# Kernel optimization log

Measured on AMD Instinct MI355X. Metric: run time of the kernel, lower is better.

The kernel has to match this reference:

```python
import jax, jax.numpy as jnp
import numpy as np

D, H, E, K, DF = 1024, 16, 8, 2, 4096
HD = D // H


def setup_inputs() -> dict:
    key = jax.random.key(0)
    ks = jax.random.split(key, 16)
    s = 0.02
    return {
        "x": jax.random.normal(ks[0], (8, 1024, D), jnp.float32),
        "ln1_g": jnp.ones((D,), jnp.float32),
        "ln1_b": jnp.zeros((D,), jnp.float32),
        "Wqkv": jax.random.normal(ks[1], (D, 3 * D), jnp.float32) * s,
        "bqkv": jnp.zeros((3 * D,), jnp.float32),
        "Wo": jax.random.normal(ks[2], (D, D), jnp.float32) * s,
        "bo": jnp.zeros((D,), jnp.float32),
        "ln2_g": jnp.ones((D,), jnp.float32),
        "ln2_b": jnp.zeros((D,), jnp.float32),
        "Wr": jax.random.normal(ks[3], (D, E), jnp.float32) * s,
        "W1": jax.random.normal(ks[4], (E, D, DF), jnp.float32) * s,
        "b1": jnp.zeros((E, DF), jnp.float32),
        "W2": jax.random.normal(ks[5], (E, DF, D), jnp.float32) * s,
        "b2": jnp.zeros((E, D), jnp.float32),
    }


def _ln(x, g, b, eps=1e-5):
    mu = jnp.mean(x, axis=-1, keepdims=True)
    var = jnp.var(x, axis=-1, keepdims=True)
    return (x - mu) * jax.lax.rsqrt(var + eps) * g + b


def reference(x, ln1_g, ln1_b, Wqkv, bqkv, Wo, bo, ln2_g, ln2_b, Wr, W1, b1, W2, b2):
    B, S, _ = x.shape
    # ---- pre-norm multi-head attention ----
    n1 = _ln(x, ln1_g, ln1_b)
    qkv = n1 @ Wqkv + bqkv  # [B,S,3D]
    q, k, v = jnp.split(qkv, 3, axis=-1)
    q = q.reshape(B, S, H, HD).transpose(0, 2, 1, 3)
    k = k.reshape(B, S, H, HD).transpose(0, 2, 1, 3)
    v = v.reshape(B, S, H, HD).transpose(0, 2, 1, 3)
    scores = jnp.einsum("bhqd,bhkd->bhqk", q, k) / np.sqrt(HD).astype(np.float32)
    attn = jax.nn.softmax(scores, axis=-1)
    ao = jnp.einsum("bhqk,bhkd->bhqd", attn, v)
    ao = ao.transpose(0, 2, 1, 3).reshape(B, S, D) @ Wo + bo
    x = x + ao  # residual (dropout=0)

    # ---- pre-norm MoE FFN ----
    n2 = _ln(x, ln2_g, ln2_b).reshape(B * S, D)  # [T,D]
    logits = n2 @ Wr  # [T,E]
    probs = jax.nn.softmax(logits, axis=-1)
    topv, topi = jax.lax.top_k(probs, K)  # [T,K]
    topv = topv / jnp.sum(topv, axis=-1, keepdims=True)
    onehot = jax.nn.one_hot(topi, E, dtype=probs.dtype)  # [T,K,E]
    gates = jnp.einsum("tke,tk->te", onehot, topv)  # dense sparse gates [T,E]

    # dense dispatch: each expert's FFN weighted by its gate (zero for unrouted)
    moe = jnp.zeros_like(n2)
    for e in range(E):
        h = jax.nn.gelu(n2 @ W1[e] + b1[e])
        moe = moe + gates[:, e:e + 1] * (h @ W2[e] + b2[e])
    x = x + moe.reshape(B, S, D)

    # load-balancing aux loss: E * sum(frac_routed_e * mean_prob_e)
    frac = jnp.mean(jnp.sum(onehot, axis=1), axis=0) / K  # [E]
    aux = E * jnp.sum(frac * jnp.mean(probs, axis=0))
    return x, aux
```

## Files before the change

kernel.cpp:

```cpp
#include <hip/hip_runtime.h>
#include <cstdint>
#include <cstddef>

using u16 = unsigned short;
using u32 = unsigned int;
typedef __attribute__((ext_vector_type(8))) short bf16x8;
typedef __attribute__((ext_vector_type(4))) float f32x4;

#define T_TOK 8192
#define SEQ   1024
#define NHEAD 16

__device__ __forceinline__ u16 f2b(float f) {
  u32 u = __float_as_uint(f);
  u32 r = (u + 0x7FFFu + ((u >> 16) & 1u)) >> 16;
  return (u16)r;
}
__device__ __forceinline__ float b2f(u16 u) {
  return __uint_as_float(((u32)u) << 16);
}
__device__ __forceinline__ u32 pk_bf16(float a, float b) {
  u32 r;
  asm("v_cvt_pk_bf16_f32 %0, %1, %2" : "=v"(r) : "v"(a), "v"(b));
  return r;
}

__global__ __launch_bounds__(256)
void k_cast_transpose(const float* __restrict__ in, u16* __restrict__ out, int R, int C) {
  __shared__ float tile[32][33];
  int bc = blockIdx.x * 32, br = blockIdx.y * 32;
  size_t bofs = (size_t)blockIdx.z * R * C;
  in += bofs; out += bofs;
  int tx = threadIdx.x, ty = threadIdx.y;
  for (int i = 0; i < 32; i += 8)
    tile[ty + i][tx] = in[(size_t)(br + ty + i) * C + bc + tx];
  __syncthreads();
  for (int i = 0; i < 32; i += 8)
    out[(size_t)(bc + ty + i) * R + br + tx] = f2b(tile[tx][ty + i]);
}

__global__ __launch_bounds__(256)
void k_ln(const float* __restrict__ x, const float* __restrict__ g, const float* __restrict__ b,
          u16* __restrict__ out) {
  int row = blockIdx.x, t = threadIdx.x;
  float4 v = ((const float4*)(x + (size_t)row * 1024))[t];
  float s  = v.x + v.y + v.z + v.w;
  float ss = v.x * v.x + v.y * v.y + v.z * v.z + v.w * v.w;
  for (int d = 1; d < 64; d <<= 1) { s += __shfl_xor(s, d); ss += __shfl_xor(ss, d); }
  __shared__ float sm[8];
  int w = t >> 6, lane = t & 63;
  if (lane == 0) { sm[w] = s; sm[4 + w] = ss; }
  __syncthreads();
  s = sm[0] + sm[1] + sm[2] + sm[3];
  ss = sm[4] + sm[5] + sm[6] + sm[7];
  float mu = s * (1.f / 1024.f);
  float var = ss * (1.f / 1024.f) - mu * mu;
  float inv = rsqrtf(var + 1e-5f);
  float4 gv = ((const float4*)g)[t];
  float4 bv = ((const float4*)b)[t];
  u32 lo = pk_bf16((v.x - mu) * inv * gv.x + bv.x, (v.y - mu) * inv * gv.y + bv.y);
  u32 hi = pk_bf16((v.z - mu) * inv * gv.z + bv.z, (v.w - mu) * inv * gv.w + bv.w);
  u32* dst = (u32*)(out + (size_t)row * 1024 + t * 4);
  dst[0] = lo; dst[1] = hi;
}

template<int MODE, bool EXPERT, bool GATHER>
__global__ __launch_bounds__(256)
void k_gemm(const u16* __restrict__ A, const u16* __restrict__ BT,
            const float* __restrict__ bias, const float* __restrict__ res,
            void* __restrict__ Cout, int M, int N, int Kd, int ldA,
            const int* __restrict__ off, const int* __restrict__ rows) {
  int nx = gridDim.x, ny = gridDim.y;
  int rid = blockIdx.x + nx * (blockIdx.y + ny * blockIdx.z);
  int z, bx, by;
  if (EXPERT) {
    z = rid & 7;
    int inner = rid >> 3;
    by = inner % ny;
    bx = inner / ny;
  } else {
    z = 0;
    int xcd = rid & 7;
    int inner = rid >> 3;
    bx = inner % nx;
    by = (inner / nx) * 8 + xcd;
  }
  int m_base = 0, M_local = M;
  if (EXPERT) { m_base = off[z]; M_local = off[z + 1] - m_base; }
  if (by * 128 >= M_local) return;
  if (EXPERT) { BT += (size_t)z * N * Kd; bias += (size_t)z * N; }

  __shared__ alignas(1024) u16 As[2][4096];
  __shared__ alignas(1024) u16 Bs[2][4096];

  int t = threadIdx.x;
  int lane = t & 63, w = t >> 6;
  int wm = w >> 1, wn = w & 1;
  int lr = lane & 15;
  int slot = lane >> 4;
  int sx = (slot ^ ((lr >> 1) & 3)) << 3;

  int ssrc = (lane & 3) ^ ((lane >> 3) & 3);
  const u16* aG[2]; const u16* bG[2];
  u16* aL[2]; u16* bL[2];
#pragma unroll
  for (int c = 0; c < 2; c++) {
    int chunk = 2 * w + c;
    int rl = chunk * 16 + (lane >> 2);
    int mr = by * 128 + rl;
    int mc = mr < M_local - 1 ? mr : M_local - 1;
    size_t arow = GATHER ? (size_t)rows[m_base + mc] : (size_t)(m_base + mc);
    aG[c] = A + arow * (size_t)ldA + ssrc * 8;
    bG[c] = BT + (size_t)(bx * 128 + rl) * Kd + ssrc * 8;
    aL[c] = &As[0][chunk * 512];
    bL[c] = &Bs[0][chunk * 512];
  }

  auto stage = [&](int k0, int buf) {
#pragma unroll
    for (int c = 0; c < 2; c++) {
      __builtin_amdgcn_global_load_lds(
          (const __attribute__((address_space(1))) void*)(aG[c] + k0),
          (__attribute__((address_space(3))) void*)(aL[c] + buf * 4096), 16, 0, 0);
      __builtin_amdgcn_global_load_lds(
          (const __attribute__((address_space(1))) void*)(bG[c] + k0),
          (__attribute__((address_space(3))) void*)(bL[c] + buf * 4096), 16, 0, 0);
    }
  };

  f32x4 acc[4][4] = {};

  stage(0, 0);
  __syncthreads();
  int cur = 0;
  for (int k0 = 0; k0 < Kd; k0 += 32) {
    if (k0 + 32 < Kd) stage(k0 + 32, cur ^ 1);
    bf16x8 af[4], bfr[4];
#pragma unroll
    for (int m = 0; m < 4; m++)
      af[m] = *(const bf16x8*)&As[cur][(wm * 64 + m * 16 + lr) * 32 + sx];
#pragma unroll
    for (int n = 0; n < 4; n++)
      bfr[n] = *(const bf16x8*)&Bs[cur][(wn * 64 + n * 16 + lr) * 32 + sx];
#pragma unroll
    for (int m = 0; m < 4; m++)
#pragma unroll
      for (int n = 0; n < 4; n++)
        acc[m][n] = __builtin_amdgcn_mfma_f32_16x16x32_bf16(af[m], bfr[n], acc[m][n], 0, 0, 0);
    __syncthreads();
    cur ^= 1;
  }

  int cr = (lane >> 4) * 4, cc = lane & 15;
#pragma unroll
  for (int m = 0; m < 4; m++) {
    int rl = by * 128 + wm * 64 + m * 16 + cr;
#pragma unroll
    for (int n = 0; n < 4; n++) {
      int col = bx * 128 + wn * 64 + n * 16 + cc;
      float bia = bias[col];
      float v0 = acc[m][n][0] + bia, v1 = acc[m][n][1] + bia;
      float v2 = acc[m][n][2] + bia, v3 = acc[m][n][3] + bia;
      if (MODE == 2) {
        const float cc2 = -2.3025850929940457f;
        float u0 = v0 + 0.044715f * v0 * v0 * v0;
        float u1 = v1 + 0.044715f * v1 * v1 * v1;
        float u2 = v2 + 0.044715f * v2 * v2 * v2;
        float u3 = v3 + 0.044715f * v3 * v3 * v3;
        v0 = v0 / (1.f + exp2f(cc2 * u0));
        v1 = v1 / (1.f + exp2f(cc2 * u1));
        v2 = v2 / (1.f + exp2f(cc2 * u2));
        v3 = v3 / (1.f + exp2f(cc2 * u3));
      }
      if (MODE == 0 || MODE == 2) {
        u32 p01 = pk_bf16(v0, v1), p23 = pk_bf16(v2, v3);
        u16* cp = (u16*)Cout;
        if (rl + 0 < M_local) cp[(size_t)(m_base + rl + 0) * N + col] = (u16)p01;
        if (rl + 1 < M_local) cp[(size_t)(m_base + rl + 1) * N + col] = (u16)(p01 >> 16);
        if (rl + 2 < M_local) cp[(size_t)(m_base + rl + 2) * N + col] = (u16)p23;
        if (rl + 3 < M_local) cp[(size_t)(m_base + rl + 3) * N + col] = (u16)(p23 >> 16);
      } else {
        float* cp = (float*)Cout;
        float vv[4] = {v0, v1, v2, v3};
#pragma unroll
        for (int r = 0; r < 4; r++) {
          int rr = rl + r;
          if (rr >= M_local) continue;
          size_t row = (size_t)(m_base + rr);
          if (MODE == 1) cp[row * N + col] = vv[r] + res[row * N + col];
          else           cp[row * N + col] = vv[r];
        }
      }
    }
  }
}

__global__ __launch_bounds__(256)
void k_attn(const u16* __restrict__ qkv, u16* __restrict__ ao) {
  __shared__ u16 Kt[64][72];
  __shared__ u16 Vt[64][72];
  __shared__ u16 Pl[4][16][72];

  int bh = blockIdx.y;
  int b = bh >> 4, h = bh & 15;
  int q0 = blockIdx.x * 64;
  int t = threadIdx.x, lane = t & 63, w = t >> 6;
  int lr = lane & 15, lk = (lane >> 4) * 8;

  int tq = b * SEQ + q0 + w * 16 + lr;
  const u16* qrow = qkv + (size_t)tq * 3072 + h * 64;
  bf16x8 qf[2];
#pragma unroll
  for (int kk = 0; kk < 2; kk++) {
    bf16x8 raw = *(const bf16x8*)(qrow + kk * 32 + lk);
#pragma unroll
    for (int j = 0; j < 8; j++) raw[j] = (short)f2b(b2f((u16)raw[j]) * 0.125f);
    qf[kk] = raw;
  }

  float m[4], l[4];
  f32x4 o[4];
#pragma unroll
  for (int r = 0; r < 4; r++) { m[r] = -1e30f; l[r] = 0.f; }
#pragma unroll
  for (int c = 0; c < 4; c++) o[c] = (f32x4){0.f, 0.f, 0.f, 0.f};

  int key_r = t >> 2;
  int key_c = (t & 3) * 16;

  for (int kv0 = 0; kv0 < SEQ; kv0 += 64) {
    int tk = b * SEQ + kv0 + key_r;
    const u16* krow = qkv + (size_t)tk * 3072 + 1024 + h * 64 + key_c;
    const u16* vrow = qkv + (size_t)tk * 3072 + 2048 + h * 64 + key_c;
    int4 ka = *(const int4*)krow;
    int4 kb = *(const int4*)(krow + 8);
    int4 vv4[2];
    vv4[0] = *(const int4*)vrow;
    vv4[1] = *(const int4*)(vrow + 8);
    const u16* vv = (const u16*)vv4;
    __syncthreads();
    *(int4*)&Kt[key_r][key_c] = ka;
    *(int4*)&Kt[key_r][key_c + 8] = kb;
#pragma unroll
    for (int j = 0; j < 16; j++) Vt[key_c + j][key_r] = vv[j];
    __syncthreads();

    f32x4 s[4];
#pragma unroll
    for (int n = 0; n < 4; n++) {
      s[n] = (f32x4){0.f, 0.f, 0.f, 0.f};
#pragma unroll
      for (int kk = 0; kk < 2; kk++) {
        bf16x8 kf = *(const bf16x8*)&Kt[n * 16 + lr][kk * 32 + lk];
        s[n] = __builtin_amdgcn_mfma_f32_16x16x32_bf16(qf[kk], kf, s[n], 0, 0, 0);
      }
    }
    float alpha[4], rsum[4];
#pragma unroll
    for (int r = 0; r < 4; r++) {
      float mx = fmaxf(fmaxf(s[0][r], s[1][r]), fmaxf(s[2][r], s[3][r]));
#pragma unroll
      for (int d = 1; d < 16; d <<= 1) mx = fmaxf(mx, __shfl_xor(mx, d));
      float mn = fmaxf(m[r], mx);
      alpha[r] = expf(m[r] - mn);
      m[r] = mn;
      rsum[r] = 0.f;
    }
#pragma unroll
    for (int n = 0; n < 4; n++)
#pragma unroll
      for (int r = 0; r < 4; r++) {
        float p = expf(s[n][r] - m[r]);
        rsum[r] += p;
        Pl[w][(lane >> 4) * 4 + r][n * 16 + lr] = f2b(p);
      }
#pragma unroll
    for (int r = 0; r < 4; r++) {
      float rs = rsum[r];
#pragma unroll
      for (int d = 1; d < 16; d <<= 1) rs += __shfl_xor(rs, d);
      l[r] = l[r] * alpha[r] + rs;
#pragma unroll
      for (int c = 0; c < 4; c++) o[c][r] *= alpha[r];
    }
    bf16x8 pa[2];
#pragma unroll
    for (int kk = 0; kk < 2; kk++) pa[kk] = *(const bf16x8*)&Pl[w][lr][kk * 32 + lk];
#pragma unroll
    for (int c = 0; c < 4; c++)
#pragma unroll
      for (int kk = 0; kk < 2; kk++) {
        bf16x8 vf = *(const bf16x8*)&Vt[c * 16 + lr][kk * 32 + lk];
        o[c] = __builtin_amdgcn_mfma_f32_16x16x32_bf16(pa[kk], vf, o[c], 0, 0, 0);
      }
  }

  int cr = (lane >> 4) * 4, cc = lane & 15;
#pragma unroll
  for (int r = 0; r < 4; r++) {
    float invl = 1.f / l[r];
    int trow = b * SEQ + q0 + w * 16 + cr + r;
#pragma unroll
    for (int c = 0; c < 4; c++)
      ao[(size_t)trow * 1024 + h * 64 + c * 16 + cc] = f2b(o[c][r] * invl);
  }
}

__global__ __launch_bounds__(256)
void k_router(const float* __restrict__ x1, const float* __restrict__ g, const float* __restrict__ b,
              const float* __restrict__ Wr, u16* __restrict__ n2b,
              int* __restrict__ topi, float* __restrict__ topv,
              int* __restrict__ cnt_part, float* __restrict__ sp_part) {
  __shared__ int lcnt[8];
  __shared__ float lsp[8];
  int t = threadIdx.x, w = t >> 6, lane = t & 63;
  if (t < 8) { lcnt[t] = 0; lsp[t] = 0.f; }
  __syncthreads();

  float gv[16], bv[16];
#pragma unroll
  for (int i = 0; i < 4; i++) {
    float4 g4 = ((const float4*)g)[lane * 4 + i];
    float4 b4 = ((const float4*)b)[lane * 4 + i];
    gv[i * 4 + 0] = g4.x; gv[i * 4 + 1] = g4.y; gv[i * 4 + 2] = g4.z; gv[i * 4 + 3] = g4.w;
    bv[i * 4 + 0] = b4.x; bv[i * 4 + 1] = b4.y; bv[i * 4 + 2] = b4.z; bv[i * 4 + 3] = b4.w;
  }
  float wr[16][8];
#pragma unroll
  for (int j = 0; j < 16; j++) {
    float4 w0 = ((const float4*)Wr)[(lane * 16 + j) * 2];
    float4 w1 = ((const float4*)Wr)[(lane * 16 + j) * 2 + 1];
    wr[j][0] = w0.x; wr[j][1] = w0.y; wr[j][2] = w0.z; wr[j][3] = w0.w;
    wr[j][4] = w1.x; wr[j][5] = w1.y; wr[j][6] = w1.z; wr[j][7] = w1.w;
  }

  for (int i = 0; i < 8; i++) {
    int row = blockIdx.x * 32 + w * 8 + i;
    const float4* xr = (const float4*)(x1 + (size_t)row * 1024);
    float xv[16];
    float s = 0.f, ss = 0.f;
#pragma unroll
    for (int q = 0; q < 4; q++) {
      float4 v = xr[lane * 4 + q];
      xv[q * 4 + 0] = v.x; xv[q * 4 + 1] = v.y; xv[q * 4 + 2] = v.z; xv[q * 4 + 3] = v.w;
      s += v.x + v.y + v.z + v.w;
      ss += v.x * v.x + v.y * v.y + v.z * v.z + v.w * v.w;
    }
#pragma unroll
    for (int d = 1; d < 64; d <<= 1) { s += __shfl_xor(s, d); ss += __shfl_xor(ss, d); }
    float mu = s * (1.f / 1024.f);
    float var = ss * (1.f / 1024.f) - mu * mu;
    float inv = rsqrtf(var + 1e-5f);
    float p[8] = {};
#pragma unroll
    for (int j = 0; j < 16; j++) {
      float n = (xv[j] - mu) * inv * gv[j] + bv[j];
      xv[j] = n;
#pragma unroll
      for (int e = 0; e < 8; e++) p[e] += n * wr[j][e];
    }
    {
      u32 pk[8];
#pragma unroll
      for (int jj = 0; jj < 8; jj++) pk[jj] = pk_bf16(xv[2 * jj], xv[2 * jj + 1]);
      uint4* dst = (uint4*)(n2b + (size_t)row * 1024 + lane * 16);
      dst[0] = make_uint4(pk[0], pk[1], pk[2], pk[3]);
      dst[1] = make_uint4(pk[4], pk[5], pk[6], pk[7]);
    }
#pragma unroll
    for (int e = 0; e < 8; e++)
#pragma unroll
      for (int d = 1; d < 64; d <<= 1) p[e] += __shfl_xor(p[e], d);
    if (lane == 0) {
      float mx = p[0];
#pragma unroll
      for (int e = 1; e < 8; e++) mx = fmaxf(mx, p[e]);
      float ex[8], sum = 0.f;
#pragma unroll
      for (int e = 0; e < 8; e++) { ex[e] = expf(p[e] - mx); sum += ex[e]; }
      float pr[8];
#pragma unroll
      for (int e = 0; e < 8; e++) pr[e] = ex[e] / sum;
      int i0 = 0; float b0 = pr[0];
      for (int e = 1; e < 8; e++) if (pr[e] > b0) { b0 = pr[e]; i0 = e; }
      int i1 = -1; float b1 = -1.f;
      for (int e = 0; e < 8; e++) if (e != i0 && pr[e] > b1) { b1 = pr[e]; i1 = e; }
      float inv2 = 1.f / (b0 + b1);
      topi[row * 2] = i0; topi[row * 2 + 1] = i1;
      topv[row * 2] = b0 * inv2; topv[row * 2 + 1] = b1 * inv2;
      atomicAdd(&lcnt[i0], 1); atomicAdd(&lcnt[i1], 1);
#pragma unroll
      for (int e = 0; e < 8; e++) atomicAdd(&lsp[e], pr[e]);
    }
  }
  __syncthreads();
  if (t < 8) {
    cnt_part[blockIdx.x * 8 + t] = lcnt[t];
    sp_part[blockIdx.x * 8 + t] = lsp[t];
  }
}

__global__ void k_scan_aux(const int* __restrict__ cnt_part, const float* __restrict__ sp_part,
                           int* __restrict__ off, int* __restrict__ cursor, float* __restrict__ aux_out) {
  __shared__ int csum[8];
  __shared__ float ssum[8];
  int t = threadIdx.x;
  int e = t & 7, ch = t >> 3;
  int c = 0; float s = 0.f;
  for (int i = ch * 32; i < ch * 32 + 32; i++) { c += cnt_part[i * 8 + e]; s += sp_part[i * 8 + e]; }
#pragma unroll
  for (int d = 8; d < 64; d <<= 1) { c += __shfl_xor(c, d); s += __shfl_xor(s, d); }
  if (t < 8) { csum[t] = c; ssum[t] = s; }
  __syncthreads();
  if (t == 0) {
    int o = 0;
    for (int q = 0; q < 8; q++) { off[q] = o; cursor[q] = o; o += csum[q]; }
    off[8] = o;
    float aux = 0.f;
    for (int q = 0; q < 8; q++)
      aux += ((float)csum[q] / (float)(T_TOK * 2)) * (ssum[q] / (float)T_TOK);
    aux_out[0] = 8.f * aux;
  }
}

__global__ __launch_bounds__(256)
void k_scatter(const int* __restrict__ topi, int* __restrict__ cursor,
               int* __restrict__ rows, int* __restrict__ slot_of) {
  __shared__ int hist[8];
  __shared__ int base[8];
  int t = threadIdx.x;
  if (t < 8) hist[t] = 0;
  __syncthreads();
  int tok = blockIdx.x * 256 + t;
  int e0 = topi[tok * 2], e1 = topi[tok * 2 + 1];
  int r0 = atomicAdd(&hist[e0], 1);
  int r1 = atomicAdd(&hist[e1], 1);
  __syncthreads();
  if (t < 8) base[t] = atomicAdd(&cursor[t], hist[t]);
  __syncthreads();
  int p0 = base[e0] + r0, p1 = base[e1] + r1;
  rows[p0] = tok; rows[p1] = tok;
  slot_of[tok * 2] = p0; slot_of[tok * 2 + 1] = p1;
}

__global__ __launch_bounds__(256)
void k_combine(const float* __restrict__ x1, const u16* __restrict__ out2,
               const int* __restrict__ slot_of, const float* __restrict__ topv,
               float* __restrict__ out) {
  int row = blockIdx.x, t = threadIdx.x;
  int s0 = slot_of[row * 2], s1 = slot_of[row * 2 + 1];
  float w0 = topv[row * 2], w1 = topv[row * 2 + 1];
  float4 a = ((const float4*)(x1 + (size_t)row * 1024))[t];
  ushort4 e0 = ((const ushort4*)(out2 + (size_t)s0 * 1024))[t];
  ushort4 e1 = ((const ushort4*)(out2 + (size_t)s1 * 1024))[t];
  float4 r;
  r.x = a.x + w0 * b2f(e0.x) + w1 * b2f(e1.x);
  r.y = a.y + w0 * b2f(e0.y) + w1 * b2f(e1.y);
  r.z = a.z + w0 * b2f(e0.z) + w1 * b2f(e1.z);
  r.w = a.w + w0 * b2f(e0.w) + w1 * b2f(e1.w);
  ((float4*)(out + (size_t)row * 1024))[t] = r;
}

extern "C" void kernel_launch(void* const* d_in, const int* in_sizes, int n_in,
                              void* d_out, int out_size, void* d_ws, size_t ws_size,
                              hipStream_t stream) {
  const float* x    = (const float*)d_in[0];
  const float* ln1g = (const float*)d_in[1];
  const float* ln1b = (const float*)d_in[2];
  const float* Wqkv = (const float*)d_in[3];
  const float* bqkv = (const float*)d_in[4];
  const float* Wo   = (const float*)d_in[5];
  const float* bo   = (const float*)d_in[6];
  const float* ln2g = (const float*)d_in[7];
  const float* ln2b = (const float*)d_in[8];
  const float* Wr   = (const float*)d_in[9];
  const float* W1   = (const float*)d_in[10];
  const float* b1   = (const float*)d_in[11];
  const float* W2   = (const float*)d_in[12];
  const float* b2   = (const float*)d_in[13];
  float* out = (float*)d_out;

  char* wp = (char*)d_ws;
  auto alloc = [&](size_t bytes) -> void* {
    void* p = (void*)wp;
    wp += (bytes + 255) & ~(size_t)255;
    return p;
  };
  u16*   WqkvT = (u16*)alloc((size_t)3072 * 1024 * 2);
  u16*   WoT   = (u16*)alloc((size_t)1024 * 1024 * 2);
  u16*   W1T   = (u16*)alloc((size_t)8 * 4096 * 1024 * 2);
  u16*   W2T   = (u16*)alloc((size_t)8 * 1024 * 4096 * 2);
  u16*   n1    = (u16*)alloc((size_t)8192 * 1024 * 2);
  u16*   qkv   = (u16*)alloc((size_t)8192 * 3072 * 2);
  u16*   aob   = (u16*)alloc((size_t)8192 * 1024 * 2);
  float* x1    = (float*)alloc((size_t)8192 * 1024 * 4);
  u16*   n2b   = (u16*)alloc((size_t)8192 * 1024 * 2);
  u16*   hbuf  = (u16*)alloc((size_t)16384 * 4096 * 2);
  u16*   out2  = (u16*)alloc((size_t)16384 * 1024 * 2);
  int*   topi  = (int*)alloc((size_t)8192 * 2 * 4);
  float* topv  = (float*)alloc((size_t)8192 * 2 * 4);
  int*   rowsl = (int*)alloc((size_t)16384 * 4);
  int*   slot  = (int*)alloc((size_t)16384 * 4);
  int*   cntp  = (int*)alloc((size_t)256 * 8 * 4);
  float* spp   = (float*)alloc((size_t)256 * 8 * 4);
  int*   offs  = (int*)alloc(256);
  int*   curs  = (int*)alloc(256);

  k_cast_transpose<<<dim3(96, 32, 1), dim3(32, 8), 0, stream>>>(Wqkv, WqkvT, 1024, 3072);
  k_cast_transpose<<<dim3(32, 32, 1), dim3(32, 8), 0, stream>>>(Wo, WoT, 1024, 1024);
  k_cast_transpose<<<dim3(128, 32, 8), dim3(32, 8), 0, stream>>>(W1, W1T, 1024, 4096);
  k_cast_transpose<<<dim3(32, 128, 8), dim3(32, 8), 0, stream>>>(W2, W2T, 4096, 1024);

  k_ln<<<8192, 256, 0, stream>>>(x, ln1g, ln1b, n1);
  k_gemm<0, false, false><<<dim3(24, 64, 1), 256, 0, stream>>>(
      n1, WqkvT, bqkv, nullptr, qkv, 8192, 3072, 1024, 1024, nullptr, nullptr);
  k_attn<<<dim3(16, 128), 256, 0, stream>>>(qkv, aob);
  k_gemm<1, false, false><<<dim3(8, 64, 1), 256, 0, stream>>>(
      aob, WoT, bo, x, x1, 8192, 1024, 1024, 1024, nullptr, nullptr);

  k_router<<<256, 256, 0, stream>>>(x1, ln2g, ln2b, Wr, n2b, topi, topv, cntp, spp);
  k_scan_aux<<<1, 64, 0, stream>>>(cntp, spp, offs, curs, out + 8388608);
  k_scatter<<<32, 256, 0, stream>>>(topi, curs, rowsl, slot);

  k_gemm<2, true, true><<<dim3(32, 64, 8), 256, 0, stream>>>(
      n2b, W1T, b1, nullptr, hbuf, 0, 4096, 1024, 1024, offs, rowsl);
  k_gemm<0, true, false><<<dim3(8, 64, 8), 256, 0, stream>>>(
      hbuf, W2T, b2, nullptr, out2, 0, 1024, 4096, 4096, offs, nullptr);
  k_combine<<<8192, 256, 0, stream>>>(x1, out2, slot, topv, out);
}
```

Before: 882.0 us.

## Add dedicated 256x256-tile grouped FFN1 GEMM kernel with fused GELU

Replaces the generic grouped GEMM for the first expert FFN layer with a specialized kernel. It uses 512 threads, a 256x256 output tile, and double-buffered direct global-to-LDS loads with a swizzled layout. Block IDs are remapped so the expert index varies fastest, to spread experts across CUs. GELU is fused into the epilogue using a tanh form written as a sigmoid through exp2. The larger tile is meant to raise arithmetic intensity and cut LDS/global traffic per FLOP. In exchange it raises register pressure (128 accumulator floats per thread) and wastes more work on padded tiles when an expert gets few tokens.

Result: slower. 956.6 us (+8.5%).

```diff
diff --git a/kernel.cpp b/kernel.cpp
--- a/kernel.cpp
+++ b/kernel.cpp
@@ -195,6 +195,110 @@
   }
 }
 
+__global__ __launch_bounds__(512, 2)
+void k_ffn1_256(const u16* __restrict__ A, const u16* __restrict__ BT,
+                const float* __restrict__ bias, u16* __restrict__ Cout,
+                int N, int Kd, int ldA,
+                const int* __restrict__ off, const int* __restrict__ rows) {
+  int nx = gridDim.x, ny = gridDim.y;
+  int rid = blockIdx.x + nx * (blockIdx.y + ny * blockIdx.z);
+  int z = rid & 7;
+  int inner = rid >> 3;
+  int by = inner % ny;
+  int bx = inner / ny;
+  int m_base = off[z];
+  int M_local = off[z + 1] - m_base;
+  if (by * 256 >= M_local) return;
+  BT += (size_t)z * N * Kd;
+  bias += (size_t)z * N;
+
+  __shared__ alignas(1024) u16 As[2][8192];
+  __shared__ alignas(1024) u16 Bs[2][8192];
+
+  int t = threadIdx.x;
+  int lane = t & 63, w = t >> 6;
+  int wm = w >> 2, wn = w & 3;
+  int lr = lane & 15;
+  int slot = lane >> 4;
+  int sx = (slot ^ ((lr >> 1) & 3)) << 3;
+
+  int ssrc = (t & 3) ^ ((t >> 3) & 3);
+  const u16* aG[2]; const u16* bG[2];
+  int lofs[2];
+#pragma unroll
+  for (int p = 0; p < 2; p++) {
+    int rl = p * 128 + (t >> 2);
+    int mr = by * 256 + rl;
+    int mc = mr < M_local - 1 ? mr : M_local - 1;
+    size_t arow = (size_t)rows[m_base + mc];
+    aG[p] = A + arow * (size_t)ldA + ssrc * 8;
+    bG[p] = BT + (size_t)(bx * 256 + rl) * Kd + ssrc * 8;
+    lofs[p] = p * 4096 + w * 512;
+  }
+
+  auto stage = [&](int k0, int buf) {
+#pragma unroll
+    for (int p = 0; p < 2; p++) {
+      __builtin_amdgcn_global_load_lds(
+          (const __attribute__((address_space(1))) void*)(aG[p] + k0),
+          (__attribute__((address_space(3))) void*)(&As[buf][lofs[p]]), 16, 0, 0);
+      __builtin_amdgcn_global_load_lds(
+          (const __attribute__((address_space(1))) void*)(bG[p] + k0),
+          (__attribute__((address_space(3))) void*)(&Bs[buf][lofs[p]]), 16, 0, 0);
+    }
+  };
+
+  f32x4 acc[8][4] = {};
+
+  stage(0, 0);
+  __syncthreads();
+  int cur = 0;
+  for (int k0 = 0; k0 < Kd; k0 += 32) {
+    if (k0 + 32 < Kd) stage(k0 + 32, cur ^ 1);
+    bf16x8 af[8], bfr[4];
+#pragma unroll
+    for (int m = 0; m < 8; m++)
+      af[m] = *(const bf16x8*)&As[cur][(wm * 128 + m * 16 + lr) * 32 + sx];
+#pragma unroll
+    for (int n = 0; n < 4; n++)
+      bfr[n] = *(const bf16x8*)&Bs[cur][(wn * 64 + n * 16 + lr) * 32 + sx];
+#pragma unroll
+    for (int m = 0; m < 8; m++)
+#pragma unroll
+      for (int n = 0; n < 4; n++)
+        acc[m][n] = __builtin_amdgcn_mfma_f32_16x16x32_bf16(af[m], bfr[n], acc[m][n], 0, 0, 0);
+    __syncthreads();
+    cur ^= 1;
+  }
+
+  int cr = (lane >> 4) * 4, cc = lane & 15;
+#pragma unroll
+  for (int m = 0; m < 8; m++) {
+    int rl = by * 256 + wm * 128 + m * 16 + cr;
+#pragma unroll
+    for (int n = 0; n < 4; n++) {
+      int col = bx * 256 + wn * 64 + n * 16 + cc;
+      float bia = bias[col];
+      float v0 = acc[m][n][0] + bia, v1 = acc[m][n][1] + bia;
+      float v2 = acc[m][n][2] + bia, v3 = acc[m][n][3] + bia;
+      const float cc2 = -2.3025850929940457f;
+      float u0 = v0 + 0.044715f * v0 * v0 * v0;
+      float u1 = v1 + 0.044715f * v1 * v1 * v1;
+      float u2 = v2 + 0.044715f * v2 * v2 * v2;
+      float u3 = v3 + 0.044715f * v3 * v3 * v3;
+      v0 = v0 / (1.f + exp2f(cc2 * u0));
+      v1 = v1 / (1.f + exp2f(cc2 * u1));
+      v2 = v2 / (1.f + exp2f(cc2 * u2));
+      v3 = v3 / (1.f + exp2f(cc2 * u3));
+      u32 p01 = pk_bf16(v0, v1), p23 = pk_bf16(v2, v3);
+      if (rl + 0 < M_local) Cout[(size_t)(m_base + rl + 0) * N + col] = (u16)p01;
+      if (rl + 1 < M_local) Cout[(size_t)(m_base + rl + 1) * N + col] = (u16)(p01 >> 16);
+      if (rl + 2 < M_local) Cout[(size_t)(m_base + rl + 2) * N + col] = (u16)p23;
+      if (rl + 3 < M_local) Cout[(size_t)(m_base + rl + 3) * N + col] = (u16)(p23 >> 16);
+    }
+  }
+}
+
 __global__ __launch_bounds__(256)
 void k_attn(const u16* __restrict__ qkv, u16* __restrict__ ao) {
   __shared__ u16 Kt[64][72];
@@ -522,8 +626,8 @@
   k_scan_aux<<<1, 64, 0, stream>>>(cntp, spp, offs, curs, out + 8388608);
   k_scatter<<<32, 256, 0, stream>>>(topi, curs, rowsl, slot);
 
-  k_gemm<2, true, true><<<dim3(32, 64, 8), 256, 0, stream>>>(
-      n2b, W1T, b1, nullptr, hbuf, 0, 4096, 1024, 1024, offs, rowsl);
+  k_ffn1_256<<<dim3(16, 32, 8), 512, 0, stream>>>(
+      n2b, W1T, b1, hbuf, 4096, 1024, 1024, offs, rowsl);
   k_gemm<0, true, false><<<dim3(8, 64, 8), 256, 0, stream>>>(
       hbuf, W2T, b2, nullptr, out2, 0, 1024, 4096, 4096, offs, nullptr);
   k_combine<<<8192, 256, 0, stream>>>(x1, out2, slot, topv, out);
```
